# Optimization experiments

Measured on AMD Instinct MI355X. Metric: run time of the kernel, lower is better.

The kernel has to match this reference:

```python
import jax, jax.numpy as jnp
import numpy as np

B, T, D, H = 2, 2048, 1024, 16
HD = D // H  # head_dim = 64


def setup_inputs() -> dict:
    key = jax.random.key(0)
    ks = jax.random.split(key, 5)
    s = 0.02
    return {
        "x": jax.random.normal(ks[0], (B, T, D), dtype=jnp.float32),
        "Wqkv": jax.random.normal(ks[1], (3 * D, D), dtype=jnp.float32) * s,
        "bqkv": jax.random.normal(ks[2], (3 * D,), dtype=jnp.float32) * s,
        "Wproj": jax.random.normal(ks[3], (D, D), dtype=jnp.float32) * s,
        "bproj": jax.random.normal(ks[4], (D,), dtype=jnp.float32) * s,
    }


def reference(x, Wqkv, bqkv, Wproj, bproj):
    b, t, d = x.shape
    qkv = x @ Wqkv.T + bqkv                      # [B,T,3D]
    q, k, v = jnp.split(qkv, 3, axis=-1)
    # [B,T,D] -> [B,H,T,HD]
    def to_heads(u):
        return u.reshape(b, t, H, HD).transpose(0, 2, 1, 3)
    q, k, v = to_heads(q), to_heads(k), to_heads(v)
    scale = 1.0 / jnp.sqrt(jnp.float32(HD))
    attn = jnp.einsum("bhqd,bhkd->bhqk", q, k) * scale   # [B,H,T,T]
    causal = jnp.tril(jnp.ones((t, t), dtype=bool))
    attn = jnp.where(causal[None, None, :, :], attn, -jnp.inf)
    attn = jax.nn.softmax(attn, axis=-1)
    scores = jnp.einsum("bhqk,bhkd->bhqd", attn, v)       # [B,H,T,HD]
    scores = scores.transpose(0, 2, 1, 3).reshape(b, t, d)
    return scores @ Wproj.T + bproj
```

## Files before the change

### kernel.cpp

```cpp
#include <hip/hip_runtime.h>

typedef __bf16 bf16_8 __attribute__((ext_vector_type(8)));
typedef __bf16 bf16_4 __attribute__((ext_vector_type(4)));
typedef __bf16 bf16_2 __attribute__((ext_vector_type(2)));
typedef float  f32_4  __attribute__((ext_vector_type(4)));
typedef float  f32_16 __attribute__((ext_vector_type(16)));

typedef __attribute__((address_space(1))) const void* as1_cvp;
typedef __attribute__((address_space(3))) void*       as3_vp;

__device__ __forceinline__ void load16_to_lds(const void* g, void* l) {
    __builtin_amdgcn_global_load_lds((as1_cvp)g, (as3_vp)l, 16, 0, 0);
}

__device__ __forceinline__ float fast_exp2(float x) {
#if __has_builtin(__builtin_amdgcn_exp2f)
    return __builtin_amdgcn_exp2f(x);
#else
    return exp2f(x);
#endif
}

__device__ __forceinline__ unsigned pk2(float lo, float hi) {
    union { bf16_2 h; unsigned u; } t;
    t.h = bf16_2{(__bf16)lo, (__bf16)hi};
    return t.u;
}

__device__ __forceinline__ void pswap(unsigned &a, unsigned &b) {
    asm("v_permlane32_swap_b32 %0, %1" : "+v"(a), "+v"(b));
}

__global__ __launch_bounds__(256) void cvt_all(
    const float* __restrict__ a, const float* __restrict__ b,
    const float* __restrict__ c, __bf16* __restrict__ out,
    int na4, int nb4, int nc4)
{
    int i = blockIdx.x * 256 + threadIdx.x;
    if (i >= na4 + nb4 + nc4) return;
    float4 f;
    if (i < na4)            f = ((const float4*)a)[i];
    else if (i < na4 + nb4) f = ((const float4*)b)[i - na4];
    else                    f = ((const float4*)c)[i - na4 - nb4];
    bf16_4 v = { (__bf16)f.x, (__bf16)f.y, (__bf16)f.z, (__bf16)f.w };
    ((bf16_4*)out)[i] = v;
}

#define BM 128

template<int OUT_BF16, int BN_, int QKV, int PIPE>
__global__ __launch_bounds__(256) void gemm_bt(
    const __bf16* __restrict__ A,
    const __bf16* __restrict__ B,
    const float*  __restrict__ bias,
    __bf16* __restrict__ Cb, float* __restrict__ Cf,
    __bf16* __restrict__ Vtb,
    int M, int N, int K, int ldc)
{
    constexpr int NT   = BN_ / 32;
    constexpr int CSTR = BN_ + (OUT_BF16 ? 8 : 4);
    constexpr int BUFB = (128 * 64 + BN_ * 64) * 2;
    constexpr int SMEMSZ = PIPE ? (3 * BUFB) : 35840;
    __shared__ __align__(16) char smem[SMEMSZ];

    const int tid  = threadIdx.x;
    const int wave = tid >> 6;
    const int lane = tid & 63;
    const int wm = wave >> 1, wn = wave & 1;
    const int quad = lane >> 4, l16 = lane & 15;
    const int bm = blockIdx.y * BM, bn = blockIdx.x * BN_;

    const int r0 = tid >> 3;
    const int ch = tid & 7;
    const int cs = (ch ^ (r0 & 7)) * 8;

    f32_4 acc[4][NT];
    #pragma unroll
    for (int i = 0; i < 4; ++i)
        #pragma unroll
        for (int j = 0; j < NT; ++j)
            acc[i][j] = f32_4{0.f, 0.f, 0.f, 0.f};

    if constexpr (!PIPE) {
        __bf16* As = (__bf16*)smem;
        __bf16* Bs = As + 128 * 64;
        for (int k0 = 0; k0 < K; k0 += 64) {
            __syncthreads();
            #pragma unroll
            for (int p = 0; p < 4; ++p) {
                int row = p * 32 + r0;
                load16_to_lds(A + (size_t)(bm + row) * K + k0 + cs,
                              &As[(p * 32 + wave * 8) * 64]);
            }
            #pragma unroll
            for (int p = 0; p < BN_ / 32; ++p) {
                int row = p * 32 + r0;
                load16_to_lds(B + (size_t)(bn + row) * K + k0 + cs,
                              &Bs[(p * 32 + wave * 8) * 64]);
            }
            __syncthreads();

            #pragma unroll
            for (int h = 0; h < 2; ++h) {
                const int sl = ((quad + h * 4) ^ (l16 & 7)) * 8;
                bf16_8 af[4], bfr[NT];
                #pragma unroll
                for (int mt = 0; mt < 4; ++mt)
                    af[mt] = *(const bf16_8*)&As[(wm * 64 + mt * 16 + l16) * 64 + sl];
                #pragma unroll
                for (int nt = 0; nt < NT; ++nt)
                    bfr[nt] = *(const bf16_8*)&Bs[(wn * (BN_/2) + nt * 16 + l16) * 64 + sl];
                #pragma unroll
                for (int mt = 0; mt < 4; ++mt)
                    #pragma unroll
                    for (int nt = 0; nt < NT; ++nt)
                        acc[mt][nt] = __builtin_amdgcn_mfma_f32_16x16x32_bf16(
                            af[mt], bfr[nt], acc[mt][nt], 0, 0, 0);
            }
        }
    } else {
        const int nit = K / 64;
        #pragma unroll
        for (int t = 0; t < 2; ++t) {
            __bf16* AsT = (__bf16*)(smem + t * BUFB);
            __bf16* BsT = AsT + 128 * 64;
            #pragma unroll
            for (int p = 0; p < 4; ++p)
                load16_to_lds(A + (size_t)(bm + p * 32 + r0) * K + t * 64 + cs,
                              &AsT[(p * 32 + wave * 8) * 64]);
            #pragma unroll
            for (int p = 0; p < BN_ / 32; ++p)
                load16_to_lds(B + (size_t)(bn + p * 32 + r0) * K + t * 64 + cs,
                              &BsT[(p * 32 + wave * 8) * 64]);
        }
        int cur = 0, sb = 2;
        for (int j = 0; j < nit; ++j) {
            if (j < nit - 1) asm volatile("s_waitcnt vmcnt(6)" ::: "memory");
            else             asm volatile("s_waitcnt vmcnt(0)" ::: "memory");
            __builtin_amdgcn_s_barrier();

            if (j + 2 < nit) {
                const int k0 = (j + 2) * 64;
                __bf16* AsT = (__bf16*)(smem + sb * BUFB);
                __bf16* BsT = AsT + 128 * 64;
                #pragma unroll
                for (int p = 0; p < 4; ++p)
                    load16_to_lds(A + (size_t)(bm + p * 32 + r0) * K + k0 + cs,
                                  &AsT[(p * 32 + wave * 8) * 64]);
                #pragma unroll
                for (int p = 0; p < BN_ / 32; ++p)
                    load16_to_lds(B + (size_t)(bn + p * 32 + r0) * K + k0 + cs,
                                  &BsT[(p * 32 + wave * 8) * 64]);
            }

            __bf16* As = (__bf16*)(smem + cur * BUFB);
            __bf16* Bs = As + 128 * 64;
            #pragma unroll
            for (int h = 0; h < 2; ++h) {
                const int sl = ((quad + h * 4) ^ (l16 & 7)) * 8;
                bf16_8 af[4], bfr[NT];
                #pragma unroll
                for (int mt = 0; mt < 4; ++mt)
                    af[mt] = *(const bf16_8*)&As[(wm * 64 + mt * 16 + l16) * 64 + sl];
                #pragma unroll
                for (int nt = 0; nt < NT; ++nt)
                    bfr[nt] = *(const bf16_8*)&Bs[(wn * (BN_/2) + nt * 16 + l16) * 64 + sl];
                #pragma unroll
                for (int mt = 0; mt < 4; ++mt)
                    #pragma unroll
                    for (int nt = 0; nt < NT; ++nt)
                        acc[mt][nt] = __builtin_amdgcn_mfma_f32_16x16x32_bf16(
                            af[mt], bfr[nt], acc[mt][nt], 0, 0, 0);
            }
            cur = (cur == 2) ? 0 : cur + 1;
            sb  = (sb  == 2) ? 0 : sb  + 1;
        }
    }

    if (QKV && bn >= 2048) {
        const int b_ = bm >> 11;
        const int t0 = (bm & 2047) + wm * 64;
        #pragma unroll
        for (int nt = 0; nt < NT; ++nt) {
            int vrow = (bn - 2048) + wn * (BN_/2) + nt * 16 + l16;
            float bv = bias ? bias[2048 + vrow] : 0.f;
            #pragma unroll
            for (int mt = 0; mt < 4; ++mt) {
                bf16_4 ov;
                #pragma unroll
                for (int r = 0; r < 4; ++r)
                    ov[r] = (__bf16)(acc[mt][nt][r] + bv);
                *(bf16_4*)(Vtb + ((size_t)b_ * 1024 + vrow) * 2048
                           + t0 + mt * 16 + quad * 4) = ov;
            }
        }
        return;
    }

    __syncthreads();

    if (OUT_BF16) {
        __bf16* Cs = (__bf16*)smem;
        #pragma unroll
        for (int mt = 0; mt < 4; ++mt)
            #pragma unroll
            for (int nt = 0; nt < NT; ++nt) {
                int col = wn * (BN_/2) + nt * 16 + l16;
                float bv = bias ? bias[bn + col] : 0.f;
                #pragma unroll
                for (int r = 0; r < 4; ++r)
                    Cs[(wm * 64 + mt * 16 + quad * 4 + r) * CSTR + col] =
                        (__bf16)(acc[mt][nt][r] + bv);
            }
        __syncthreads();
        const int rr = tid >> 4, cc = (tid & 15) * 8;
        #pragma unroll
        for (int p = 0; p < 8; ++p) {
            int row = p * 16 + rr;
            bf16_8 v = *(const bf16_8*)&Cs[row * CSTR + cc];
            *(bf16_8*)(Cb + (size_t)(bm + row) * ldc + bn + cc) = v;
        }
    } else {
        float* Cs = (float*)smem;
        #pragma unroll
        for (int mt = 0; mt < 4; ++mt)
            #pragma unroll
            for (int nt = 0; nt < NT; ++nt) {
                int col = wn * (BN_/2) + nt * 16 + l16;
                float bv = bias ? bias[bn + col] : 0.f;
                #pragma unroll
                for (int r = 0; r < 4; ++r)
                    Cs[(wm * 64 + mt * 16 + quad * 4 + r) * CSTR + col] =
                        acc[mt][nt][r] + bv;
            }
        __syncthreads();
        const int rr = tid >> 4, cc = (tid & 15) * 4;
        #pragma unroll
        for (int p = 0; p < 8; ++p) {
            int row = p * 16 + rr;
            float4 v = *(const float4*)&Cs[row * CSTR + cc];
            *(float4*)(Cf + (size_t)(bm + row) * ldc + bn + cc) = v;
        }
    }
}

__global__ __launch_bounds__(256, 2) void attn_kernel(
    const __bf16* __restrict__ qk, const __bf16* __restrict__ vt,
    __bf16* __restrict__ out)
{
    constexpr int T = 2048;
    __shared__ __align__(16) char pool[49152];
    __bf16* Ks = (__bf16*)pool;
    __bf16* Vt = (__bf16*)(pool + 24576);
    float*  Om = (float*)pool;
    float*  Lm = (float*)(pool + 34816);

    const int tid  = threadIdx.x;
    const int wave = tid >> 6;
    const int lane = tid & 63;
    const int wq = wave & 1, wg = wave >> 1;
    const int l32 = lane & 31, hh = lane >> 5;

    const int fid  = blockIdx.x;
    const int xcd  = fid & 7;
    const int hsel = fid >> 8;
    const int w    = (fid >> 3) & 31;
    const int qt   = hsel ? (7 - (w >> 2)) : ((w >> 2) + 8);
    const int bh   = xcd * 4 + (w & 3);
    const int b = bh >> 4, h = bh & 15;
    const int jmax = 2 * qt + 1;

    const size_t rowbase = (size_t)b * T;
    const __bf16* Kbase = qk + 1024 + h * 64;
    const __bf16* Vbase = vt + (size_t)bh * 64 * 2048;

    const int sr   = tid >> 3;
    const int schf = (tid & 7) ^ (sr & 7);

    constexpr float QSCALE = 0.125f * 1.4426950408889634f;
    bf16_8 aq[2][4];
    #pragma unroll
    for (int qq = 0; qq < 2; ++qq)
        #pragma unroll
        for (int df = 0; df < 4; ++df) {
            const __bf16* qp = qk + (rowbase + qt*128 + wq*64 + qq*32 + l32)*2048
                               + h*64 + df*16 + hh*8;
            bf16_8 v = *(const bf16_8*)qp;
            #pragma unroll
            for (int u = 0; u < 8; ++u) v[u] = (__bf16)((float)v[u] * QSCALE);
            aq[qq][df] = v;
        }

    #pragma unroll
    for (int t0 = 0; t0 < 2; ++t0)
        #pragma unroll
        for (int p = 0; p < 2; ++p) {
            load16_to_lds(Kbase + (rowbase + t0*64 + sr + 32*p)*2048 + schf*8,
                          Ks + t0*4096 + p*2048 + wave*512);
            load16_to_lds(Vbase + (size_t)(sr + 32*p)*2048 + t0*64 + schf*8,
                          Vt + t0*4096 + p*2048 + wave*512);
        }

    f32_16 O[2][2];
    #pragma unroll
    for (int dt = 0; dt < 2; ++dt)
        #pragma unroll
        for (int qq = 0; qq < 2; ++qq)
            #pragma unroll
            for (int r = 0; r < 16; ++r) O[dt][qq][r] = 0.f;
    float l_i[2] = {0.f, 0.f};

    int cur = 0;
    int sb  = 2;
    for (int j = 0; j <= jmax; ++j) {
        if (j < jmax) asm volatile("s_waitcnt vmcnt(4)" ::: "memory");
        else          asm volatile("s_waitcnt vmcnt(0)" ::: "memory");
        __builtin_amdgcn_s_barrier();

        const int jn = j + 2;
        if (jn <= jmax) {
            #pragma unroll
            for (int p = 0; p < 2; ++p) {
                load16_to_lds(Kbase + (rowbase + jn*64 + sr + 32*p)*2048 + schf*8,
                              Ks + sb*4096 + p*2048 + wave*512);
                load16_to_lds(Vbase + (size_t)(sr + 32*p)*2048 + jn*64 + schf*8,
                              Vt + sb*4096 + p*2048 + wave*512);
            }
        }

        const int krow = wg*32 + l32;
        const int ksw  = krow & 7;
        f32_16 S[2];
        __builtin_amdgcn_s_setprio(1);
        bf16_8 kf[4];
        #pragma unroll
        for (int df = 0; df < 4; ++df)
            kf[df] = *(const bf16_8*)&Ks[cur*4096 + krow*64 + (((2*df + hh) ^ ksw) << 3)];
        #pragma unroll
        for (int qq = 0; qq < 2; ++qq) {
            f32_16 z;
            #pragma unroll
            for (int r = 0; r < 16; ++r) z[r] = 0.f;
            #pragma unroll
            for (int df = 0; df < 4; ++df)
                z = __builtin_amdgcn_mfma_f32_32x32x16_bf16(kf[df], aq[qq][df], z, 0, 0, 0);
            S[qq] = z;
        }
        __builtin_amdgcn_s_setprio(0);

        const bool diag = (j >= 2*qt);
        unsigned fr[2][8];
        #pragma unroll
        for (int qq = 0; qq < 2; ++qq) {
            float pe[16];
            const int qg = qt*128 + wq*64 + qq*32 + l32;
            #pragma unroll
            for (int r = 0; r < 16; ++r) {
                float e = fast_exp2(S[qq][r]);
                if (diag) {
                    int key = j*64 + wg*32 + (r&3) + 8*(r>>2) + 4*hh;
                    if (key > qg) e = 0.f;
                }
                pe[r] = e;
                l_i[qq] += e;
            }
            unsigned A = pk2(pe[0],  pe[1]),  Bv = pk2(pe[2],  pe[3]),
                     C = pk2(pe[4],  pe[5]),  D  = pk2(pe[6],  pe[7]),
                     E = pk2(pe[8],  pe[9]),  F  = pk2(pe[10], pe[11]),
                     G = pk2(pe[12], pe[13]), H  = pk2(pe[14], pe[15]);
            pswap(A, C); pswap(Bv, D); pswap(E, G); pswap(F, H);
            fr[qq][0] = A; fr[qq][1] = Bv; fr[qq][2] = C; fr[qq][3] = D;
            fr[qq][4] = E; fr[qq][5] = F;  fr[qq][6] = G; fr[qq][7] = H;
        }

        __builtin_amdgcn_s_setprio(1);
        #pragma unroll
        for (int kh = 0; kh < 2; ++kh) {
            #pragma unroll
            for (int dt = 0; dt < 2; ++dt) {
                const int d = dt*32 + l32;
                bf16_8 vf = *(const bf16_8*)&Vt[cur*4096 + d*64 +
                                (((wg*4 + kh*2 + hh) ^ (d & 7)) << 3)];
                #pragma unroll
                for (int qq = 0; qq < 2; ++qq) {
                    union { unsigned dw[4]; bf16_8 v; } u;
                    u.dw[0] = fr[qq][kh*4+0]; u.dw[1] = fr[qq][kh*4+1];
                    u.dw[2] = fr[qq][kh*4+2]; u.dw[3] = fr[qq][kh*4+3];
                    O[dt][qq] = __builtin_amdgcn_mfma_f32_32x32x16_bf16(
                        vf, u.v, O[dt][qq], 0, 0, 0);
                }
            }
        }
        __builtin_amdgcn_s_setprio(0);

        cur = (cur == 2) ? 0 : cur + 1;
        sb  = (sb  == 2) ? 0 : sb  + 1;
    }

    float lw[2];
    #pragma unroll
    for (int qq = 0; qq < 2; ++qq) {
        float v = l_i[qq];
        v += __shfl_xor(v, 32, 64);
        lw[qq] = v;
    }

    __syncthreads();
    if (wg == 1) {
        #pragma unroll
        for (int qq = 0; qq < 2; ++qq) {
            const int qrow = wq*64 + qq*32 + l32;
            #pragma unroll
            for (int dt = 0; dt < 2; ++dt)
                #pragma unroll
                for (int g = 0; g < 4; ++g) {
                    f32_4 t = { O[dt][qq][g*4+0], O[dt][qq][g*4+1],
                                O[dt][qq][g*4+2], O[dt][qq][g*4+3] };
                    *(f32_4*)&Om[qrow*68 + dt*32 + g*8 + hh*4] = t;
                }
            if (hh == 0) Lm[qrow] = lw[qq];
        }
    }
    __syncthreads();
    if (wg == 0) {
        #pragma unroll
        for (int qq = 0; qq < 2; ++qq) {
            const int qrow = wq*64 + qq*32 + l32;
            const float inv = 1.f / (lw[qq] + Lm[qrow]);
            const size_t obase = (rowbase + qt*128 + qrow) * 1024 + h*64;
            #pragma unroll
            for (int dt = 0; dt < 2; ++dt)
                #pragma unroll
                for (int g = 0; g < 4; ++g) {
                    f32_4 o2 = *(const f32_4*)&Om[qrow*68 + dt*32 + g*8 + hh*4];
                    bf16_4 ov;
                    #pragma unroll
                    for (int r = 0; r < 4; ++r)
                        ov[r] = (__bf16)((O[dt][qq][g*4+r] + o2[r]) * inv);
                    *(bf16_4*)(out + obase + dt*32 + g*8 + hh*4) = ov;
                }
        }
    }
}

extern "C" void kernel_launch(void* const* d_in, const int* in_sizes, int n_in,
                              void* d_out, int out_size, void* d_ws, size_t ws_size,
                              hipStream_t stream)
{
    constexpr int Bc = 2, Tc = 2048, Dc = 1024;
    constexpr int M  = Bc * Tc;
    constexpr int N1 = 3 * Dc;

    const float* x     = (const float*)d_in[0];
    const float* Wqkv  = (const float*)d_in[1];
    const float* bqkv  = (const float*)d_in[2];
    const float* Wproj = (const float*)d_in[3];
    const float* bproj = (const float*)d_in[4];
    float* outp = (float*)d_out;

    __bf16* xb     = (__bf16*)d_ws;
    __bf16* wqkvb  = xb     + (size_t)M * Dc;
    __bf16* wprojb = wqkvb  + (size_t)N1 * Dc;
    __bf16* qkb    = wprojb + (size_t)Dc * Dc;
    __bf16* vtb    = qkb    + (size_t)M * 2048;
    __bf16* attnb  = vtb    + (size_t)Bc * 1024 * 2048;

    {
        int na4 = M * Dc / 4, nb4 = N1 * Dc / 4, nc4 = Dc * Dc / 4;
        int n4 = na4 + nb4 + nc4;
        cvt_all<<<(n4 + 255) / 256, 256, 0, stream>>>(x, Wqkv, Wproj, xb, na4, nb4, nc4);
    }

    gemm_bt<1, 128, 1, 0><<<dim3(N1 / 128, M / BM), 256, 0, stream>>>(
        xb, wqkvb, bqkv, qkb, nullptr, vtb, M, N1, Dc, 2048);

    attn_kernel<<<dim3(512), 256, 0, stream>>>(qkb, vtb, attnb);

    gemm_bt<0, 64, 0, 1><<<dim3(Dc / 64, M / BM), 256, 0, stream>>>(
        attnb, wprojb, bproj, nullptr, outp, nullptr, M, Dc, Dc, Dc);
}
```

Baseline: 162.8 us.

## Switch attention K/V staging to double-buffered 128-key tiles with half the barriers

```diff
diff --git a/kernel.cpp b/kernel.cpp
--- a/kernel.cpp
+++ b/kernel.cpp
@@ -249,9 +249,8 @@
     __bf16* __restrict__ out)
 {
     constexpr int T = 2048;
-    __shared__ __align__(16) char pool[49152];
+    __shared__ __align__(16) char pool[65536];
     __bf16* Ks = (__bf16*)pool;
-    __bf16* Vt = (__bf16*)(pool + 24576);
     float*  Om = (float*)pool;
     float*  Lm = (float*)(pool + 34816);
 
@@ -268,7 +267,6 @@
     const int qt   = hsel ? (7 - (w >> 2)) : ((w >> 2) + 8);
     const int bh   = xcd * 4 + (w & 3);
     const int b = bh >> 4, h = bh & 15;
-    const int jmax = 2 * qt + 1;
 
     const size_t rowbase = (size_t)b * T;
     const __bf16* Kbase = qk + 1024 + h * 64;
@@ -292,13 +290,13 @@
         }
 
     #pragma unroll
-    for (int t0 = 0; t0 < 2; ++t0)
+    for (int sub = 0; sub < 2; ++sub)
         #pragma unroll
         for (int p = 0; p < 2; ++p) {
-            load16_to_lds(Kbase + (rowbase + t0*64 + sr + 32*p)*2048 + schf*8,
-                          Ks + t0*4096 + p*2048 + wave*512);
-            load16_to_lds(Vbase + (size_t)(sr + 32*p)*2048 + t0*64 + schf*8,
-                          Vt + t0*4096 + p*2048 + wave*512);
+            load16_to_lds(Kbase + (rowbase + sub*64 + sr + 32*p)*2048 + schf*8,
+                          Ks + sub*4096 + p*2048 + wave*512);
+            load16_to_lds(Vbase + (size_t)(sr + 32*p)*2048 + sub*64 + schf*8,
+                          Ks + 8192 + sub*4096 + p*2048 + wave*512);
         }
 
     f32_16 O[2][2];
@@ -310,91 +308,95 @@
             for (int r = 0; r < 16; ++r) O[dt][qq][r] = 0.f;
     float l_i[2] = {0.f, 0.f};
 
-    int cur = 0;
-    int sb  = 2;
-    for (int j = 0; j <= jmax; ++j) {
-        if (j < jmax) asm volatile("s_waitcnt vmcnt(4)" ::: "memory");
-        else          asm volatile("s_waitcnt vmcnt(0)" ::: "memory");
+    const int krow = wg*32 + l32;
+    const int ksw  = krow & 7;
+
+    for (int j = 0; j <= qt; ++j) {
+        const int cur = j & 1, nxt = cur ^ 1;
+        asm volatile("s_waitcnt vmcnt(0)" ::: "memory");
         __builtin_amdgcn_s_barrier();
 
-        const int jn = j + 2;
-        if (jn <= jmax) {
-            #pragma unroll
-            for (int p = 0; p < 2; ++p) {
-                load16_to_lds(Kbase + (rowbase + jn*64 + sr + 32*p)*2048 + schf*8,
-                              Ks + sb*4096 + p*2048 + wave*512);
-                load16_to_lds(Vbase + (size_t)(sr + 32*p)*2048 + jn*64 + schf*8,
-                              Vt + sb*4096 + p*2048 + wave*512);
-            }
-        }
-
-        const int krow = wg*32 + l32;
-        const int ksw  = krow & 7;
-        f32_16 S[2];
-        __builtin_amdgcn_s_setprio(1);
-        bf16_8 kf[4];
-        #pragma unroll
-        for (int df = 0; df < 4; ++df)
-            kf[df] = *(const bf16_8*)&Ks[cur*4096 + krow*64 + (((2*df + hh) ^ ksw) << 3)];
-        #pragma unroll
-        for (int qq = 0; qq < 2; ++qq) {
-            f32_16 z;
-            #pragma unroll
-            for (int r = 0; r < 16; ++r) z[r] = 0.f;
+        if (j < qt) {
+            const int jn = j + 1;
+            #pragma unroll
+            for (int sub = 0; sub < 2; ++sub)
+                #pragma unroll
+                for (int p = 0; p < 2; ++p) {
+                    load16_to_lds(Kbase + (rowbase + jn*128 + sub*64 + sr + 32*p)*2048 + schf*8,
+                                  Ks + nxt*16384 + sub*4096 + p*2048 + wave*512);
+                    load16_to_lds(Vbase + (size_t)(sr + 32*p)*2048 + jn*128 + sub*64 + schf*8,
+                                  Ks + nxt*16384 + 8192 + sub*4096 + p*2048 + wave*512);
+                }
+        }
+
+        const bool diag = (j == qt);
+        #pragma unroll
+        for (int s2 = 0; s2 < 2; ++s2) {
+            const __bf16* Kc = Ks + cur*16384 + s2*4096;
+            const __bf16* Vc = Ks + cur*16384 + 8192 + s2*4096;
+
+            f32_16 S[2];
+            __builtin_amdgcn_s_setprio(1);
+            bf16_8 kf[4];
             #pragma unroll
             for (int df = 0; df < 4; ++df)
-                z = __builtin_amdgcn_mfma_f32_32x32x16_bf16(kf[df], aq[qq][df], z, 0, 0, 0);
-            S[qq] = z;
-        }
-        __builtin_amdgcn_s_setprio(0);
-
-        const bool diag = (j >= 2*qt);
-        unsigned fr[2][8];
-        #pragma unroll
-        for (int qq = 0; qq < 2; ++qq) {
-            float pe[16];
-            const int qg = qt*128 + wq*64 + qq*32 + l32;
-            #pragma unroll
-            for (int r = 0; r < 16; ++r) {
-                float e = fast_exp2(S[qq][r]);
-                if (diag) {
-                    int key = j*64 + wg*32 + (r&3) + 8*(r>>2) + 4*hh;
-                    if (key > qg) e = 0.f;
+                kf[df] = *(const bf16_8*)&Kc[krow*64 + (((2*df + hh) ^ ksw) << 3)];
+            #pragma unroll
+            for (int qq = 0; qq < 2; ++qq) {
+                f32_16 z;
+                #pragma unroll
+                for (int r = 0; r < 16; ++r) z[r] = 0.f;
+                #pragma unroll
+                for (int df = 0; df < 4; ++df)
+                    z = __builtin_amdgcn_mfma_f32_32x32x16_bf16(kf[df], aq[qq][df], z, 0, 0, 0);
+                S[qq] = z;
+            }
+            __builtin_amdgcn_s_setprio(0);
+
+            unsigned fr[2][8];
+            #pragma unroll
+            for (int qq = 0; qq < 2; ++qq) {
+                float pe[16];
+                const int qg = qt*128 + wq*64 + qq*32 + l32;
+                #pragma unroll
+                for (int r = 0; r < 16; ++r) {
+                    float e = fast_exp2(S[qq][r]);
+                    if (diag) {
+                        int key = j*128 + s2*64 + wg*32 + (r&3) + 8*(r>>2) + 4*hh;
+                        if (key > qg) e = 0.f;
+                    }
+                    pe[r] = e;
+                    l_i[qq] += e;
                 }
-                pe[r] = e;
-                l_i[qq] += e;
-            }
-            unsigned A = pk2(pe[0],  pe[1]),  Bv = pk2(pe[2],  pe[3]),
-                     C = pk2(pe[4],  pe[5]),  D  = pk2(pe[6],  pe[7]),
-                     E = pk2(pe[8],  pe[9]),  F  = pk2(pe[10], pe[11]),
-                     G = pk2(pe[12], pe[13]), H  = pk2(pe[14], pe[15]);
-            pswap(A, C); pswap(Bv, D); pswap(E, G); pswap(F, H);
-            fr[qq][0] = A; fr[qq][1] = Bv; fr[qq][2] = C; fr[qq][3] = D;
-            fr[qq][4] = E; fr[qq][5] = F;  fr[qq][6] = G; fr[qq][7] = H;
-        }
-
-        __builtin_amdgcn_s_setprio(1);
-        #pragma unroll
-        for (int kh = 0; kh < 2; ++kh) {
-            #pragma unroll
-            for (int dt = 0; dt < 2; ++dt) {
-                const int d = dt*32 + l32;
-                bf16_8 vf = *(const bf16_8*)&Vt[cur*4096 + d*64 +
-                                (((wg*4 + kh*2 + hh) ^ (d & 7)) << 3)];
-                #pragma unroll
-                for (int qq = 0; qq < 2; ++qq) {
-                    union { unsigned dw[4]; bf16_8 v; } u;
-                    u.dw[0] = fr[qq][kh*4+0]; u.dw[1] = fr[qq][kh*4+1];
-                    u.dw[2] = fr[qq][kh*4+2]; u.dw[3] = fr[qq][kh*4+3];
-                    O[dt][qq] = __builtin_amdgcn_mfma_f32_32x32x16_bf16(
-                        vf, u.v, O[dt][qq], 0, 0, 0);
+                unsigned A = pk2(pe[0],  pe[1]),  Bv = pk2(pe[2],  pe[3]),
+                         C = pk2(pe[4],  pe[5]),  D  = pk2(pe[6],  pe[7]),
+                         E = pk2(pe[8],  pe[9]),  F  = pk2(pe[10], pe[11]),
+                         G = pk2(pe[12], pe[13]), H  = pk2(pe[14], pe[15]);
+                pswap(A, C); pswap(Bv, D); pswap(E, G); pswap(F, H);
+                fr[qq][0] = A; fr[qq][1] = Bv; fr[qq][2] = C; fr[qq][3] = D;
+                fr[qq][4] = E; fr[qq][5] = F;  fr[qq][6] = G; fr[qq][7] = H;
+            }
+
+            __builtin_amdgcn_s_setprio(1);
+            #pragma unroll
+            for (int kh = 0; kh < 2; ++kh) {
+                #pragma unroll
+                for (int dt = 0; dt < 2; ++dt) {
+                    const int d = dt*32 + l32;
+                    bf16_8 vf = *(const bf16_8*)&Vc[d*64 +
+                                    (((wg*4 + kh*2 + hh) ^ (d & 7)) << 3)];
+                    #pragma unroll
+                    for (int qq = 0; qq < 2; ++qq) {
+                        union { unsigned dw[4]; bf16_8 v; } u;
+                        u.dw[0] = fr[qq][kh*4+0]; u.dw[1] = fr[qq][kh*4+1];
+                        u.dw[2] = fr[qq][kh*4+2]; u.dw[3] = fr[qq][kh*4+3];
+                        O[dt][qq] = __builtin_amdgcn_mfma_f32_32x32x16_bf16(
+                            vf, u.v, O[dt][qq], 0, 0, 0);
+                    }
                 }
             }
-        }
-        __builtin_amdgcn_s_setprio(0);
-
-        cur = (cur == 2) ? 0 : cur + 1;
-        sb  = (sb  == 2) ? 0 : sb  + 1;
+            __builtin_amdgcn_s_setprio(0);
+        }
     }
 
     float lw[2];
```

Result: no change. 160.6 us (-1.4%).
